# Optimization experiments

Measured on AMD Instinct MI355X. Metric: run time of the kernel, lower is better.

The kernel has to match this reference:

```python
import jax, jax.numpy as jnp
import numpy as np

B, T, C = 128, 512, 512
EPS = 1e-5


def setup_inputs() -> dict:
    key = jax.random.key(0)
    ks = jax.random.split(key, 12)
    s_tri = 1.0 / np.sqrt(T)   # rough torch Linear init scale (per-row fan-in varies; fixed for simplicity)
    s_fc1 = 1.0 / np.sqrt(C)
    s_fc2 = 1.0 / np.sqrt(2 * C)
    return {
        "inputs": jax.random.normal(ks[0], (B, T, C), dtype=jnp.float32),
        "ln1_w": jnp.ones((T, C), jnp.float32),
        "ln1_b": jnp.zeros((T, C), jnp.float32),
        "ln2_w": jnp.ones((T, C), jnp.float32),
        "ln2_b": jnp.zeros((T, C), jnp.float32),
        # Row s of triu_W corresponds to nn.Linear(s+1, 1); entries j> s are masked in reference().
        "triu_W": jax.random.uniform(ks[1], (T, T), jnp.float32, -s_tri, s_tri),
        "triu_b": jax.random.uniform(ks[2], (T,), jnp.float32, -s_tri, s_tri),
        "fc1_W": jax.random.uniform(ks[3], (2 * C, C), jnp.float32, -s_fc1, s_fc1),
        "fc1_b": jax.random.uniform(ks[4], (2 * C,), jnp.float32, -s_fc1, s_fc1),
        "fc2_W": jax.random.uniform(ks[5], (C, 2 * C), jnp.float32, -s_fc2, s_fc2),
        "fc2_b": jax.random.uniform(ks[6], (C,), jnp.float32, -s_fc2, s_fc2),
    }


def _layernorm_2d(x, w, b):
    # torch nn.LayerNorm((T, C)): normalize jointly over the last TWO dims.
    mu = jnp.mean(x, axis=(-2, -1), keepdims=True)
    var = jnp.var(x, axis=(-2, -1), keepdims=True)
    return (x - mu) * jax.lax.rsqrt(var + EPS) * w + b


def reference(inputs, ln1_w, ln1_b, ln2_w, ln2_b, triu_W, triu_b, fc1_W, fc1_b, fc2_W, fc2_b):
    x = _layernorm_2d(inputs, ln1_w, ln1_b)                       # [B,T,C]
    # TriU time mixer on x.mT ([B,C,T]): out[..., s] = sum_{t<=s} W[s,t]*x[..., t] + b[s]
    Wm = jnp.tril(triu_W)                                          # causal mask
    xm = jnp.einsum('btc,st->bsc', x, Wm) + triu_b[None, :, None]  # [B,T,C] (already back-transposed)
    x2 = _layernorm_2d(xm + inputs, ln2_w, ln2_b)                  # [B,T,C]
    h = jax.nn.gelu(jnp.einsum('btc,hc->bth', x2, fc1_W) + fc1_b, approximate=False)
    y = jnp.einsum('bth,ch->btc', h, fc2_W) + fc2_b
    return x2 + y
```

## Files before the change

kernel.cpp:

```cpp
#include <hip/hip_runtime.h>
#include <hip/hip_fp8.h>
#include <cstdint>

typedef unsigned short u16;
typedef unsigned char u8;
typedef __attribute__((ext_vector_type(8))) short s16x8;
typedef __attribute__((ext_vector_type(4))) float f32x4;
typedef __attribute__((ext_vector_type(8))) unsigned short u16x8;
typedef __attribute__((ext_vector_type(4))) unsigned short u16x4;

#define B_ 128
#define T_ 512
#define C_ 512
#define TC 262144

static __device__ __forceinline__ float bf2f(u16 u) {
  union { unsigned int i; float f; } v; v.i = ((unsigned int)u) << 16; return v.f;
}
static __device__ __forceinline__ u16 f2bf(float f) {
  union { float fv; unsigned int i; } v; v.fv = f;
  unsigned int r = (v.i + 0x7FFFu + ((v.i >> 16) & 1u)) >> 16;
  return (u16)r;
}
static __device__ __forceinline__ unsigned int cvtpk_fp8(float a, float b) {
  unsigned int r;
  asm volatile("v_cvt_pk_fp8_f32 %0, %1, %2" : "=v"(r) : "v"(a), "v"(b));
  return r & 0xffffu;
}

static __device__ __forceinline__ float gelu_fast(float x) {
  float x2 = x * x;
  float arg = 1.5957691216057308f * x * fmaf(0.044715f, x2, 1.0f);
  return x / (1.0f + __expf(-arg));
}

#define GLD16(gp, lp) __builtin_amdgcn_global_load_lds( \
    (const __attribute__((address_space(1))) void*)(gp), \
    (__attribute__((address_space(3))) void*)(lp), 16, 0, 0)


__global__ __launch_bounds__(256)
void reduce_stats_kernel(const float* __restrict__ X, float2* __restrict__ partials,
                         u16* __restrict__ Xb,
                         const float* __restrict__ triu_W, u16* __restrict__ wmb,
                         const float* __restrict__ fc1_W, u8* __restrict__ w1f8,
                         const float* __restrict__ fc2_W, u8* __restrict__ w2f8) {
  const int b = blockIdx.y, blk = blockIdx.x, tid = threadIdx.x;
  const size_t gi = (size_t)b * TC + (size_t)blk * 2048 + (size_t)tid * 8;
  const float* p = X + gi;
  f32x4 v0 = *(const f32x4*)p;
  f32x4 v1 = *(const f32x4*)(p + 4);
  float s = 0.f, q = 0.f;
  u16x8 ob;
#pragma unroll
  for (int i = 0; i < 4; ++i) {
    s += v0[i] + v1[i]; q += v0[i] * v0[i] + v1[i] * v1[i];
    ob[i] = f2bf(v0[i]); ob[4 + i] = f2bf(v1[i]);
  }
  *(u16x8*)(Xb + gi) = ob;

  const int flat = (b * 128 + blk) * 256 + tid;
  if (flat < T_ * T_) {
    const int sr = flat >> 9, tcol = flat & 511;
    wmb[flat] = f2bf(tcol <= sr ? triu_W[flat] : 0.f);
  }
  if (flat < C_ * C_) {
    float2 a1 = *(const float2*)(fc1_W + (size_t)flat * 2);
    float2 a2 = *(const float2*)(fc2_W + (size_t)flat * 2);
    *(u16*)(w1f8 + (size_t)flat * 2) = (u16)cvtpk_fp8(a1.x, a1.y);
    *(u16*)(w2f8 + (size_t)flat * 2) = (u16)cvtpk_fp8(a2.x, a2.y);
  }

  for (int o = 32; o; o >>= 1) { s += __shfl_down(s, o); q += __shfl_down(q, o); }
  __shared__ float ss[4], qq[4];
  if ((tid & 63) == 0) { ss[tid >> 6] = s; qq[tid >> 6] = q; }
  __syncthreads();
  if (tid == 0)
    partials[(size_t)b * 128 + blk] =
        make_float2(ss[0] + ss[1] + ss[2] + ss[3], qq[0] + qq[1] + qq[2] + qq[3]);
}


__global__ __launch_bounds__(256)
void ln1_transpose_kernel(const u16* __restrict__ Xb, const float* __restrict__ W,
                          const float* __restrict__ Bv, const float2* __restrict__ partials,
                          u16* __restrict__ xT) {
  const int b = blockIdx.z;
  const int t0 = blockIdx.y * 64, c0 = blockIdx.x * 64;
  const int tid = threadIdx.x;
  __shared__ u16 tile[64][72];
  __shared__ float smu, srs;

  if (tid < 64) {
    float2 p0 = partials[(size_t)b * 128 + tid];
    float2 p1 = partials[(size_t)b * 128 + 64 + tid];
    float s = p0.x + p1.x, q = p0.y + p1.y;
    for (int o = 32; o; o >>= 1) { s += __shfl_down(s, o); q += __shfl_down(q, o); }
    if (tid == 0) {
      float mean = s * (1.f / (float)TC);
      float var = q * (1.f / (float)TC) - mean * mean;
      smu = mean; srs = rsqrtf(var + 1e-5f);
    }
  }
  __syncthreads();
  const float mu = smu, rs = srs;

  const int rr = tid >> 4;
  const int cc = (tid & 15) * 4;
#pragma unroll
  for (int i = 0; i < 4; ++i) {
    const int lt = i * 16 + rr;
    const size_t wi = (size_t)(t0 + lt) * C_ + c0 + cc;
    u16x4 xa = *(const u16x4*)(Xb + (size_t)b * TC + wi);
    f32x4 w = *(const f32x4*)(W + wi);
    f32x4 bb = *(const f32x4*)(Bv + wi);
#pragma unroll
    for (int j = 0; j < 4; ++j)
      tile[lt][cc + j] = f2bf((bf2f(xa[j]) - mu) * rs * w[j] + bb[j]);
  }
  __syncthreads();
  const int c = tid >> 2;
  const int tg = (tid & 3) * 16;
  u16 buf[16];
#pragma unroll
  for (int i = 0; i < 16; ++i) buf[i] = tile[tg + i][c];
  const size_t o = (size_t)b * TC + (size_t)(c0 + c) * T_ + t0 + tg;
  u16x8 o0, o1;
#pragma unroll
  for (int i = 0; i < 8; ++i) { o0[i] = buf[i]; o1[i] = buf[8 + i]; }
  *(u16x8*)(xT + o) = o0;
  *(u16x8*)(xT + o + 8) = o1;
}


__global__ __launch_bounds__(256)
void ln2_apply_kernel(const u16* __restrict__ S, const float* __restrict__ W,
                      const float* __restrict__ Bv, const float2* __restrict__ partials2,
                      u16* __restrict__ x2, u8* __restrict__ x8) {
  const size_t i = ((size_t)blockIdx.x * 256 + threadIdx.x) * 8;
  const int b = (int)(i >> 18);
  const size_t r = i & (size_t)(TC - 1);
  float2 p0 = partials2[(size_t)b * 4 + 0];
  float2 p1 = partials2[(size_t)b * 4 + 1];
  float2 p2 = partials2[(size_t)b * 4 + 2];
  float2 p3 = partials2[(size_t)b * 4 + 3];
  float s = (p0.x + p1.x) + (p2.x + p3.x);
  float q = (p0.y + p1.y) + (p2.y + p3.y);
  const float mu = s * (1.f / (float)TC);
  const float rs = rsqrtf(q * (1.f / (float)TC) - mu * mu + 1e-5f);

  u16x8 sv = *(const u16x8*)(S + i);
  f32x4 w0 = *(const f32x4*)(W + r);
  f32x4 w1 = *(const f32x4*)(W + r + 4);
  f32x4 b0 = *(const f32x4*)(Bv + r);
  f32x4 b1 = *(const f32x4*)(Bv + r + 4);
  u16x8 o;
  float v[8];
#pragma unroll
  for (int j = 0; j < 4; ++j) {
    v[j]     = (bf2f(sv[j])     - mu) * rs * w0[j] + b0[j];
    v[4 + j] = (bf2f(sv[4 + j]) - mu) * rs * w1[j] + b1[j];
    o[j] = f2bf(v[j]); o[4 + j] = f2bf(v[4 + j]);
  }
  *(u16x8*)(x2 + i) = o;
  uint2 pk;
  pk.x = cvtpk_fp8(v[0], v[1]) | (cvtpk_fp8(v[2], v[3]) << 16);
  pk.y = cvtpk_fp8(v[4], v[5]) | (cvtpk_fp8(v[6], v[7]) << 16);
  *(uint2*)(x8 + i) = pk;
}


template <int MODE>
__global__ __launch_bounds__(512, (MODE == 0) ? 1 : 2)
void gemm_bt_kernel(const u16* __restrict__ A, const u16* __restrict__ Bm,
                    int K, int lda, int ldb,
                    void* __restrict__ Cp, int ldc,
                    const float* __restrict__ bias,
                    const void* __restrict__ res,
                    long long strideB, long long strideC,
                    float2* __restrict__ stat_part) {
  constexpr int TILE_U16 = (MODE == 0) ? 16384 : 8192;
  __shared__ u16 Asb[2 * TILE_U16];
  __shared__ u16 Bsb[2 * TILE_U16];
  __shared__ float rs_[8], rq_[8];
  const int tid = threadIdx.x;

  const int nwg = gridDim.x;
  const int orig = blockIdx.x;
  const int swz = (orig & 7) * (nwg >> 3) + (orig >> 3);
  int bx, by, bz;
  if (MODE == 0) { bz = swz >> 2; by = (swz >> 1) & 1; bx = swz & 1; }
  else if (MODE == 1) { bz = 0; by = swz >> 2; bx = swz & 3; }
  else { bz = 0; by = swz >> 1; bx = swz & 1; }

  const u16* Bp = Bm + (size_t)bz * (size_t)strideB;
  const int m0 = by * 256, n0 = bx * 256;
  int kTiles = K >> 6;
  if (MODE == 0) { const int need = (by + 1) * 4; if (need < kTiles) kTiles = need; }

  const int lane = tid & 63;
  const int wave = tid >> 6;
  const int wm = (wave >> 2) * 128;
  const int wn = (wave & 3) * 64;
  const int lr = lane & 15;
  const int kg = lane >> 4;

  f32x4 acc[8][4];
  const f32x4 zero = {0.f, 0.f, 0.f, 0.f};
#pragma unroll
  for (int m = 0; m < 8; ++m)
#pragma unroll
    for (int n = 0; n < 4; ++n) acc[m][n] = zero;

  auto STAGE_A = [&](int t) {
    const int k0 = t << 6;
    const int d = (t & 1) * 16384;
#pragma unroll
    for (int p = 0; p < 4; ++p) {
      const int q = p * 512 + tid;
      const int r = q >> 3;
      const int kcs = (q & 7) ^ (r & 7);
      GLD16(A + (size_t)(m0 + r) * lda + k0 + (kcs << 3), &Asb[d + q * 8]);
    }
  };
  auto STAGE_B = [&](int t) {
    const int k0 = t << 6;
    const int d = (t & 1) * 16384;
#pragma unroll
    for (int p = 0; p < 4; ++p) {
      const int q = p * 512 + tid;
      const int r = q >> 3;
      const int kcs = (q & 7) ^ (r & 7);
      GLD16(Bp + (size_t)(n0 + r) * ldb + k0 + (kcs << 3), &Bsb[d + q * 8]);
    }
  };
  auto STAGE_A8 = [&](int t) {
    const int k0 = t << 6;
    u8* lds = (u8*)Asb + (t & 1) * 16384;
    const u8* src = (const u8*)A;
#pragma unroll
    for (int p = 0; p < 2; ++p) {
      const int q = p * 512 + tid;
      const int lrow = q >> 3;
      const int cp = (q & 7) ^ (lrow & 7);
      const int dr = lrow + ((cp & 4) << 5);
      GLD16(src + (size_t)(m0 + dr) * lda + k0 + ((cp & 3) << 4), lds + q * 16);
    }
  };
  auto STAGE_B8 = [&](int t) {
    const int k0 = t << 6;
    u8* lds = (u8*)Bsb + (t & 1) * 16384;
    const u8* src = (const u8*)Bp;
#pragma unroll
    for (int p = 0; p < 2; ++p) {
      const int q = p * 512 + tid;
      const int lrow = q >> 3;
      const int cp = (q & 7) ^ (lrow & 7);
      const int dr = lrow + ((cp & 4) << 5);
      GLD16(src + (size_t)(n0 + dr) * ldb + k0 + ((cp & 3) << 4), lds + q * 16);
    }
  };

  if (MODE == 0) {
    STAGE_A(0); STAGE_B(0); STAGE_A(1);
    for (int kt = 0; kt < kTiles; ++kt) {
      const int d = (kt & 1) * 16384;
      if (kt + 1 < kTiles) asm volatile("s_waitcnt vmcnt(4)" ::: "memory");
      else                 asm volatile("s_waitcnt vmcnt(0)" ::: "memory");
      __builtin_amdgcn_s_barrier();
      asm volatile("" ::: "memory");

      s16x8 a0[8], a1[8], b0[4], b1[4];
#pragma unroll
      for (int m = 0; m < 8; ++m) {
        const int row = wm + m * 16 + lr;
        const u16* base = &Asb[d + row * 64];
        a0[m] = *(const s16x8*)(base + (((kg)     ^ (row & 7)) << 3));
        a1[m] = *(const s16x8*)(base + (((4 + kg) ^ (row & 7)) << 3));
      }
#pragma unroll
      for (int n = 0; n < 4; ++n) {
        const int row = wn + n * 16 + lr;
        b0[n] = *(const s16x8*)(&Bsb[d + row * 64] + (((kg) ^ (row & 7)) << 3));
      }
      if (kt + 1 < kTiles) STAGE_B(kt + 1);

      __builtin_amdgcn_s_setprio(1);
#pragma unroll
      for (int m = 0; m < 8; ++m)
#pragma unroll
        for (int n = 0; n < 4; ++n)
          acc[m][n] = __builtin_amdgcn_mfma_f32_16x16x32_bf16(a0[m], b0[n], acc[m][n], 0, 0, 0);
      __builtin_amdgcn_s_setprio(0);

#pragma unroll
      for (int n = 0; n < 4; ++n) {
        const int row = wn + n * 16 + lr;
        b1[n] = *(const s16x8*)(&Bsb[d + row * 64] + (((4 + kg) ^ (row & 7)) << 3));
      }
      asm volatile("s_waitcnt lgkmcnt(0)" ::: "memory");
      __builtin_amdgcn_s_barrier();
      asm volatile("" ::: "memory");
      if (kt + 2 < kTiles) STAGE_A(kt + 2);

      __builtin_amdgcn_s_setprio(1);
#pragma unroll
      for (int m = 0; m < 8; ++m)
#pragma unroll
        for (int n = 0; n < 4; ++n)
          acc[m][n] = __builtin_amdgcn_mfma_f32_16x16x32_bf16(a1[m], b1[n], acc[m][n], 0, 0, 0);
      __builtin_amdgcn_s_setprio(0);
    }
  } else {
    STAGE_A8(0); STAGE_B8(0); STAGE_A8(1);
    for (int kt = 0; kt < kTiles; ++kt) {
      const u8* Ad = (const u8*)Asb + (kt & 1) * 16384;
      const u8* Bd = (const u8*)Bsb + (kt & 1) * 16384;
      if (kt + 1 < kTiles) asm volatile("s_waitcnt vmcnt(2)" ::: "memory");
      else                 asm volatile("s_waitcnt vmcnt(0)" ::: "memory");
      __builtin_amdgcn_s_barrier();
      asm volatile("" ::: "memory");

      long a0[8], a1[8], b0[4], b1[4];
      const int sub = (kg & 1) * 8;
      const int hi = kg >> 1;
#pragma unroll
      for (int m = 0; m < 8; ++m) {
        const int dd = wm + m * 16 + lr;
        const int lrow = dd & 127;
        const int g4 = (dd >> 7) << 2;
        const u8* base = Ad + lrow * 128 + sub;
        a0[m] = *(const long*)(base + (((g4 | hi)       ^ (lrow & 7)) << 4));
        a1[m] = *(const long*)(base + (((g4 | (2 + hi)) ^ (lrow & 7)) << 4));
      }
#pragma unroll
      for (int n = 0; n < 4; ++n) {
        const int dd = wn + n * 16 + lr;
        const int lrow = dd & 127;
        const int g4 = (dd >> 7) << 2;
        b0[n] = *(const long*)(Bd + lrow * 128 + sub + (((g4 | hi) ^ (lrow & 7)) << 4));
      }
      if (kt + 1 < kTiles) STAGE_B8(kt + 1);

      __builtin_amdgcn_s_setprio(1);
#pragma unroll
      for (int m = 0; m < 8; ++m)
#pragma unroll
        for (int n = 0; n < 4; ++n)
          acc[m][n] = __builtin_amdgcn_mfma_f32_16x16x32_fp8_fp8(a0[m], b0[n], acc[m][n], 0, 0, 0);
      __builtin_amdgcn_s_setprio(0);

#pragma unroll
      for (int n = 0; n < 4; ++n) {
        const int dd = wn + n * 16 + lr;
        const int lrow = dd & 127;
        const int g4 = (dd >> 7) << 2;
        b1[n] = *(const long*)(Bd + lrow * 128 + sub + (((g4 | (2 + hi)) ^ (lrow & 7)) << 4));
      }
      asm volatile("s_waitcnt lgkmcnt(0)" ::: "memory");
      __builtin_amdgcn_s_barrier();
      asm volatile("" ::: "memory");
      if (kt + 2 < kTiles) STAGE_A8(kt + 2);

      __builtin_amdgcn_s_setprio(1);
#pragma unroll
      for (int m = 0; m < 8; ++m)
#pragma unroll
        for (int n = 0; n < 4; ++n)
          acc[m][n] = __builtin_amdgcn_mfma_f32_16x16x32_fp8_fp8(a1[m], b1[n], acc[m][n], 0, 0, 0);
      __builtin_amdgcn_s_setprio(0);
    }
  }

  if (MODE == 0) {
    u16* Cptr = (u16*)Cp + (size_t)bz * (size_t)strideC;
    const u16* inp = (const u16*)res + (size_t)bz * (size_t)strideC;
    float psum = 0.f, psq = 0.f;
#pragma unroll
    for (int m = 0; m < 8; ++m) {
      const int rb = m0 + wm + m * 16 + kg * 4;
#pragma unroll
      for (int n = 0; n < 4; ++n) {
        const int col = n0 + wn + n * 16 + lr;
#pragma unroll
        for (int j = 0; j < 4; ++j) {
          const size_t idx = (size_t)(rb + j) * ldc + col;
          float v = acc[m][n][j] + bf2f(inp[idx]) + bias[rb + j];
          psum += v; psq += v * v;
          Cptr[idx] = f2bf(v);
        }
      }
    }
    for (int o = 32; o; o >>= 1) { psum += __shfl_down(psum, o); psq += __shfl_down(psq, o); }
    if (lane == 0) { rs_[wave] = psum; rq_[wave] = psq; }
    __syncthreads();
    if (tid == 0) {
      float s = 0.f, q = 0.f;
#pragma unroll
      for (int w = 0; w < 8; ++w) { s += rs_[w]; q += rq_[w]; }
      stat_part[(size_t)bz * 4 + by * 2 + bx] = make_float2(s, q);
    }
  } else if (MODE == 1) {
    u8* Cptr = (u8*)Cp;
#pragma unroll
    for (int m = 0; m < 8; ++m) {
      const int rb = m0 + wm + m * 16 + kg * 4;
#pragma unroll
      for (int n = 0; n < 4; ++n) {
        const int col = n0 + wn + n * 16 + lr;
        const float bs = bias[col];
        unsigned int p01 = cvtpk_fp8(gelu_fast(acc[m][n][0] + bs),
                                     gelu_fast(acc[m][n][1] + bs));
        unsigned int p23 = cvtpk_fp8(gelu_fast(acc[m][n][2] + bs),
                                     gelu_fast(acc[m][n][3] + bs));
        Cptr[(size_t)(rb + 0) * ldc + col] = (u8)(p01 & 0xff);
        Cptr[(size_t)(rb + 1) * ldc + col] = (u8)(p01 >> 8);
        Cptr[(size_t)(rb + 2) * ldc + col] = (u8)(p23 & 0xff);
        Cptr[(size_t)(rb + 3) * ldc + col] = (u8)(p23 >> 8);
      }
    }
  } else {
    float* Cptr = (float*)Cp;
    const u16* x2p = (const u16*)res;
#pragma unroll
    for (int m = 0; m < 8; ++m) {
      const int rb = m0 + wm + m * 16 + kg * 4;
#pragma unroll
      for (int n = 0; n < 4; ++n) {
        const int col = n0 + wn + n * 16 + lr;
        const float bs = bias[col];
#pragma unroll
        for (int j = 0; j < 4; ++j) {
          const size_t idx = (size_t)(rb + j) * ldc + col;
          Cptr[idx] = acc[m][n][j] + bs + bf2f(x2p[idx]);
        }
      }
    }
  }
}


extern "C" void kernel_launch(void* const* d_in, const int* in_sizes, int n_in,
                              void* d_out, int out_size, void* d_ws, size_t ws_size,
                              hipStream_t stream) {
  const float* inputs = (const float*)d_in[0];
  const float* ln1_w  = (const float*)d_in[1];
  const float* ln1_b  = (const float*)d_in[2];
  const float* ln2_w  = (const float*)d_in[3];
  const float* ln2_b  = (const float*)d_in[4];
  const float* triu_W = (const float*)d_in[5];
  const float* triu_b = (const float*)d_in[6];
  const float* fc1_W  = (const float*)d_in[7];
  const float* fc1_b  = (const float*)d_in[8];
  const float* fc2_W  = (const float*)d_in[9];
  const float* fc2_b  = (const float*)d_in[10];
  float* out = (float*)d_out;
  (void)in_sizes; (void)n_in; (void)out_size; (void)ws_size;

  char* ws = (char*)d_ws;
  size_t off = 0;
  auto carve = [&](size_t bytes) {
    char* p = ws + off;
    off += (bytes + 255) & ~(size_t)255;
    return p;
  };
  u16* s_bf = (u16*)carve((size_t)B_ * T_ * C_ * 2);
  u16* xT   = (u16*)carve((size_t)B_ * T_ * C_ * 2);
  u16* x2   = xT;
  u16* inb  = (u16*)carve((size_t)B_ * T_ * C_ * 2);
  u8*  x8   = (u8*)carve((size_t)B_ * T_ * C_);
  u8*  h    = (u8*)carve((size_t)B_ * T_ * 2 * C_);
  u16* wmb  = (u16*)carve((size_t)T_ * T_ * 2);
  u8*  w1f8 = (u8*)carve((size_t)2 * C_ * C_);
  u8*  w2f8 = (u8*)carve((size_t)C_ * 2 * C_);
  float2* partials  = (float2*)carve(128 * 128 * sizeof(float2));
  float2* partials2 = (float2*)carve(128 * 4 * sizeof(float2));

  reduce_stats_kernel<<<dim3(128, 128), 256, 0, stream>>>(
      inputs, partials, inb, triu_W, wmb, fc1_W, w1f8, fc2_W, w2f8);
  ln1_transpose_kernel<<<dim3(8, 8, 128), 256, 0, stream>>>(inb, ln1_w, ln1_b, partials, xT);
  gemm_bt_kernel<0><<<512, 512, 0, stream>>>(
      wmb, xT, 512, 512, 512, s_bf, 512, triu_b, inb, (long long)TC, (long long)TC, partials2);
  ln2_apply_kernel<<<16384, 256, 0, stream>>>(s_bf, ln2_w, ln2_b, partials2, x2, x8);
  gemm_bt_kernel<1><<<1024, 512, 0, stream>>>(
      (const u16*)x8, (const u16*)w1f8, 512, 512, 512, h, 1024, fc1_b, nullptr, 0, 0, nullptr);
  gemm_bt_kernel<2><<<512, 512, 0, stream>>>(
      (const u16*)h, (const u16*)w2f8, 1024, 1024, 1024, out, 512, fc2_b, x2, 0, 0, nullptr);
}
```

Before: 353.3 us.

## Permute fp8 K layout so each lane loads both k-halves in one 16-byte LDS read

The fp8 GEMM operands (fc1/fc2 weights, the LN2 fp8 output, and the GELU fp8 output) are now written with a K-permutation within each 64-element group. After this, the two 8-byte fragments a lane needs for the two MFMA halves are adjacent, so the LDS reads become single 128-bit loads instead of pairs of 64-bit loads. The loads for both halves are issued up front and one lgkmcnt wait comes before the first MFMA block. In exchange, all B fragments are held in registers for the whole k-step, raising register pressure, and the GELU epilogue does byte stores to permuted columns.

```diff
diff --git a/kernel.cpp b/kernel.cpp
--- a/kernel.cpp
+++ b/kernel.cpp
@@ -8,6 +8,7 @@
 typedef __attribute__((ext_vector_type(4))) float f32x4;
 typedef __attribute__((ext_vector_type(8))) unsigned short u16x8;
 typedef __attribute__((ext_vector_type(4))) unsigned short u16x4;
+typedef __attribute__((ext_vector_type(2))) long l64x2;
 
 #define B_ 128
 #define T_ 512
@@ -26,6 +27,9 @@
   unsigned int r;
   asm volatile("v_cvt_pk_fp8_f32 %0, %1, %2" : "=v"(r) : "v"(a), "v"(b));
   return r & 0xffffu;
+}
+static __device__ __forceinline__ int kperm(int c) {
+  return (c & ~63) | (((c >> 3) & 3) << 4) | (((c >> 5) & 1) << 3) | (c & 7);
 }
 
 static __device__ __forceinline__ float gelu_fast(float x) {
@@ -65,10 +69,13 @@
     wmb[flat] = f2bf(tcol <= sr ? triu_W[flat] : 0.f);
   }
   if (flat < C_ * C_) {
-    float2 a1 = *(const float2*)(fc1_W + (size_t)flat * 2);
-    float2 a2 = *(const float2*)(fc2_W + (size_t)flat * 2);
-    *(u16*)(w1f8 + (size_t)flat * 2) = (u16)cvtpk_fp8(a1.x, a1.y);
-    *(u16*)(w2f8 + (size_t)flat * 2) = (u16)cvtpk_fp8(a2.x, a2.y);
+    const int e = flat * 2;
+    float2 a1 = *(const float2*)(fc1_W + e);
+    float2 a2 = *(const float2*)(fc2_W + e);
+    const int r1 = e >> 9,  c1 = e & 511;
+    const int r2 = e >> 10, c2 = e & 1023;
+    *(u16*)(w1f8 + (size_t)r1 * 512 + kperm(c1))  = (u16)cvtpk_fp8(a1.x, a1.y);
+    *(u16*)(w2f8 + (size_t)r2 * 1024 + kperm(c2)) = (u16)cvtpk_fp8(a2.x, a2.y);
   }
 
   for (int o = 32; o; o >>= 1) { s += __shfl_down(s, o); q += __shfl_down(q, o); }
@@ -166,7 +173,8 @@
   uint2 pk;
   pk.x = cvtpk_fp8(v[0], v[1]) | (cvtpk_fp8(v[2], v[3]) << 16);
   pk.y = cvtpk_fp8(v[4], v[5]) | (cvtpk_fp8(v[6], v[7]) << 16);
-  *(uint2*)(x8 + i) = pk;
+  const size_t pi = (i & ~(size_t)63) | (size_t)(((i >> 3) & 3) << 4) | (size_t)(((i >> 5) & 1) << 3);
+  *(uint2*)(x8 + pi) = pk;
 }
 
 
@@ -321,43 +329,32 @@
       __builtin_amdgcn_s_barrier();
       asm volatile("" ::: "memory");
 
-      long a0[8], a1[8], b0[4], b1[4];
-      const int sub = (kg & 1) * 8;
-      const int hi = kg >> 1;
+      l64x2 av[8], bv[4];
 #pragma unroll
       for (int m = 0; m < 8; ++m) {
         const int dd = wm + m * 16 + lr;
         const int lrow = dd & 127;
-        const int g4 = (dd >> 7) << 2;
-        const u8* base = Ad + lrow * 128 + sub;
-        a0[m] = *(const long*)(base + (((g4 | hi)       ^ (lrow & 7)) << 4));
-        a1[m] = *(const long*)(base + (((g4 | (2 + hi)) ^ (lrow & 7)) << 4));
+        const int q = (((dd >> 7) << 2) | kg) ^ (lrow & 7);
+        av[m] = *(const l64x2*)(Ad + lrow * 128 + (q << 4));
       }
 #pragma unroll
       for (int n = 0; n < 4; ++n) {
         const int dd = wn + n * 16 + lr;
         const int lrow = dd & 127;
-        const int g4 = (dd >> 7) << 2;
-        b0[n] = *(const long*)(Bd + lrow * 128 + sub + (((g4 | hi) ^ (lrow & 7)) << 4));
+        const int q = (((dd >> 7) << 2) | kg) ^ (lrow & 7);
+        bv[n] = *(const l64x2*)(Bd + lrow * 128 + (q << 4));
       }
       if (kt + 1 < kTiles) STAGE_B8(kt + 1);
 
+      asm volatile("s_waitcnt lgkmcnt(0)" ::: "memory");
       __builtin_amdgcn_s_setprio(1);
 #pragma unroll
       for (int m = 0; m < 8; ++m)
 #pragma unroll
         for (int n = 0; n < 4; ++n)
-          acc[m][n] = __builtin_amdgcn_mfma_f32_16x16x32_fp8_fp8(a0[m], b0[n], acc[m][n], 0, 0, 0);
+          acc[m][n] = __builtin_amdgcn_mfma_f32_16x16x32_fp8_fp8(av[m][0], bv[n][0], acc[m][n], 0, 0, 0);
       __builtin_amdgcn_s_setprio(0);
 
-#pragma unroll
-      for (int n = 0; n < 4; ++n) {
-        const int dd = wn + n * 16 + lr;
-        const int lrow = dd & 127;
-        const int g4 = (dd >> 7) << 2;
-        b1[n] = *(const long*)(Bd + lrow * 128 + sub + (((g4 | (2 + hi)) ^ (lrow & 7)) << 4));
-      }
-      asm volatile("s_waitcnt lgkmcnt(0)" ::: "memory");
       __builtin_amdgcn_s_barrier();
       asm volatile("" ::: "memory");
       if (kt + 2 < kTiles) STAGE_A8(kt + 2);
@@ -367,7 +364,7 @@
       for (int m = 0; m < 8; ++m)
 #pragma unroll
         for (int n = 0; n < 4; ++n)
-          acc[m][n] = __builtin_amdgcn_mfma_f32_16x16x32_fp8_fp8(a1[m], b1[n], acc[m][n], 0, 0, 0);
+          acc[m][n] = __builtin_amdgcn_mfma_f32_16x16x32_fp8_fp8(av[m][1], bv[n][1], acc[m][n], 0, 0, 0);
       __builtin_amdgcn_s_setprio(0);
     }
   }
@@ -409,14 +406,15 @@
       for (int n = 0; n < 4; ++n) {
         const int col = n0 + wn + n * 16 + lr;
         const float bs = bias[col];
+        const int pcol = kperm(col);
         unsigned int p01 = cvtpk_fp8(gelu_fast(acc[m][n][0] + bs),
                                      gelu_fast(acc[m][n][1] + bs));
         unsigned int p23 = cvtpk_fp8(gelu_fast(acc[m][n][2] + bs),
                                      gelu_fast(acc[m][n][3] + bs));
-        Cptr[(size_t)(rb + 0) * ldc + col] = (u8)(p01 & 0xff);
-        Cptr[(size_t)(rb + 1) * ldc + col] = (u8)(p01 >> 8);
-        Cptr[(size_t)(rb + 2) * ldc + col] = (u8)(p23 & 0xff);
-        Cptr[(size_t)(rb + 3) * ldc + col] = (u8)(p23 >> 8);
+        Cptr[(size_t)(rb + 0) * ldc + pcol] = (u8)(p01 & 0xff);
+        Cptr[(size_t)(rb + 1) * ldc + pcol] = (u8)(p01 >> 8);
+        Cptr[(size_t)(rb + 2) * ldc + pcol] = (u8)(p23 & 0xff);
+        Cptr[(size_t)(rb + 3) * ldc + pcol] = (u8)(p23 >> 8);
       }
     }
   } else {
```

Measured after the change: 337.6 us. 1.05x faster.
